# Performance work log

Hardware: AMD Instinct MI355X
Metric: run time of the kernel (lower is better)

## Reference

```python
import jax, jax.numpy as jnp
import numpy as np


def setup_inputs() -> dict:
    key = jax.random.key(0)
    ks = jax.random.split(key, 8)
    B, De, Do, T, H, W = 4, 128, 512, 4, 30, 52
    s = 0.05  # weight init scale
    return {
        "m_in": jax.random.normal(ks[0], (B, De, T, H, W), jnp.float32),
        "m_out": jax.random.normal(ks[1], (B, Do, T, H, W), jnp.float32),
        "q_in": jax.random.normal(ks[2], (B, De, H, W), jnp.float32),
        "q_out": jax.random.normal(ks[3], (B, Do, H, W), jnp.float32),
        "wr": jax.random.normal(ks[4], (Do, 2 * Do), jnp.float32) * s,
        "br": jnp.zeros((Do,), jnp.float32),
        "wu": jax.random.normal(ks[5], (Do, 2 * Do), jnp.float32) * s,
        "bu": jnp.zeros((Do,), jnp.float32),
        "wc": jax.random.normal(ks[6], (Do, 2 * Do), jnp.float32) * s,
        "bc": jnp.zeros((Do,), jnp.float32),
    }


def reference(m_in, m_out, q_in, q_out, wr, br, wu, bu, wc, bc):
    B, De, T, H, W = m_in.shape
    Do = m_out.shape[1]
    PROP_LAYERS = 5

    # --- memory read: pairwise frame attention (bmm + softmax + bmm) ---
    # keys: all T memory frames flattened; queries: current frame.
    mi = m_in.reshape(B, De, T * H * W)            # [B, De, THW]
    qi = q_in.reshape(B, De, H * W)                # [B, De, HW]
    p = jnp.einsum('bdk,bdq->bkq', mi, qi) / (De ** 0.5)  # [B, THW, HW]
    p = jax.nn.softmax(p, axis=1)                  # softmax over memory locations (dim=1 in torch)
    mem = jnp.einsum('bok,bkq->boq', m_out.reshape(B, Do, T * H * W), p)
    mem = mem.reshape(B, Do, H, W)                 # mem_mean; identical every propagate layer

    # --- ConvGRU_h (kernel_size=1 => per-pixel linear gates) ---
    def conv1x1(w, b, x):
        return jnp.einsum('oc,bchw->bohw', w, x) + b[None, :, None, None]

    def gru(x, h):
        xh = jnp.concatenate([x, h], axis=1)                       # [B, 2*Do, H, W]
        r = jax.nn.sigmoid(conv1x1(wr, br, xh))
        u = jax.nn.sigmoid(conv1x1(wu, bu, xh))
        c = jnp.tanh(conv1x1(wc, bc, jnp.concatenate([x, r * h], axis=1)))
        return h * (1.0 - u) + u * c

    q0 = q_out
    q = q_out
    for _ in range(PROP_LAYERS):
        q = gru(q, mem)  # original: q_out = ConvGRU_h(q_out, mem_mean)
    return jnp.concatenate([q, q0], axis=1)  # [B, 2*Do, H, W]
```

## Files before the change

kernel.cpp:

```cpp
#include <hip/hip_runtime.h>
#include <hip/hip_bf16.h>
#include <math.h>

typedef unsigned short u16;
typedef __attribute__((ext_vector_type(8))) short bf16x8;
typedef __attribute__((ext_vector_type(4))) float f32x4;

__device__ __forceinline__ u16 f2bf(float f) {
  union { float f; unsigned u; } x; x.f = f;
  unsigned r = x.u + 0x7fffu + ((x.u >> 16) & 1u);
  return (u16)(r >> 16);
}
__device__ __forceinline__ float bf2f(u16 h) {
  union { unsigned u; float f; } x; x.u = ((unsigned)h) << 16;
  return x.f;
}
__device__ __forceinline__ float sigmf(float x) {
  x = fminf(fmaxf(x, -30.f), 30.f);
  return 1.f / (1.f + __expf(-x));
}
__device__ __forceinline__ float tanh_fast(float x) {
  x = fminf(fmaxf(x, -15.f), 15.f);
  float t = __expf(2.f * x);
  return (t - 1.f) / (t + 1.f);
}

#define NB 4
#define DE 128
#define DO_ 512
#define HW 1560
#define THW 6240
#define NP 1664
#define KP 6272
#define PROP 5
#define PVSPLIT 7
#define PVKC 896

template<int MODE, int ROWS, int KTOT>
__global__ __launch_bounds__(256)
void gemm_ws(const u16* __restrict__ A, const u16* __restrict__ Bt,
             int lda, int ldb, long a_bs, long b_bs,
             void* __restrict__ out0v, long o0_bs, int ld0,
             u16* __restrict__ out1, long o1_bs, int ld1,
             const void* __restrict__ e0v, long e0_bs,
             const void* __restrict__ e1v, long e1_bs,
             const void* __restrict__ e2v, long e2_bs,
             int nvalid, float scale)
{
  constexpr int MF = ROWS / 16;
  constexpr int SLOTS = ROWS * KTOT / 8;
  constexpr int NLD = SLOTS / 256;
  constexpr int RSH = (ROWS == 64) ? 6 : 5;
  __shared__ u16 lds[SLOTS][8];

  const int tid = threadIdx.x;
  const int wave = tid >> 6, lane = tid & 63;
  const int kg = lane >> 4, lr = lane & 15;
  const long b = blockIdx.z;
  const int m0 = blockIdx.x * ROWS, n0 = blockIdx.y * 128;
  A += b * a_bs; Bt += b * b_bs;

  float* out0f = (float*)out0v;
  u16* out0h = (u16*)out0v;
  const float* e0f = (const float*)e0v;
  const u16* e0h = (const u16*)e0v;
  const u16* e1h = (const u16*)e1v;
  const u16* e2h = (const u16*)e2v;

#pragma unroll
  for (int i = 0; i < NLD; ++i) {
    int s = tid + 256 * i;
    int row = s & (ROWS - 1), g = s >> RSH;
    const u16* src = A + (long)(m0 + row) * lda + g * 8;
    __builtin_amdgcn_global_load_lds(
        (const __attribute__((address_space(1))) void*)src,
        (__attribute__((address_space(3))) void*)&lds[wave * 64 + 256 * i][0],
        16, 0, 0);
  }
  __syncthreads();

  f32x4 acc[MF][2];
#pragma unroll
  for (int m = 0; m < MF; ++m)
#pragma unroll
    for (int n = 0; n < 2; ++n) acc[m][n] = (f32x4){0.f, 0.f, 0.f, 0.f};

  const u16* Bp0 = Bt + (long)(n0 + wave * 32 + lr) * ldb + kg * 8;
  const u16* Bp1 = Bp0 + 16 * ldb;

  constexpr int NK = KTOT / 32;
#pragma unroll 4
  for (int g2 = 0; g2 < NK; ++g2) {
    bf16x8 af[MF], bf[2];
#pragma unroll
    for (int m = 0; m < MF; ++m)
      af[m] = *(const bf16x8*)&lds[(g2 * 4 + kg) * ROWS + m * 16 + lr][0];
    bf[0] = *(const bf16x8*)&Bp0[g2 * 32];
    bf[1] = *(const bf16x8*)&Bp1[g2 * 32];
#pragma unroll
    for (int m = 0; m < MF; ++m)
#pragma unroll
      for (int n = 0; n < 2; ++n)
        acc[m][n] = __builtin_amdgcn_mfma_f32_16x16x32_bf16(af[m], bf[n], acc[m][n], 0, 0, 0);
  }

  if constexpr (MODE == 0) {
    float rs[MF][4];
#pragma unroll
    for (int m = 0; m < MF; ++m)
#pragma unroll
      for (int j = 0; j < 4; ++j) rs[m][j] = 0.f;
#pragma unroll
    for (int m = 0; m < MF; ++m) {
#pragma unroll
      for (int n = 0; n < 2; ++n) {
        int col = n0 + wave * 32 + n * 16 + lr;
#pragma unroll
        for (int j = 0; j < 4; ++j) {
          long row = m0 + m * 16 + kg * 4 + j;
          float p = __expf(acc[m][n][j] * scale);
          bool valid = (col < nvalid);
          out1[b * o1_bs + row * ld1 + col] = valid ? f2bf(p) : (u16)0;
          rs[m][j] += valid ? p : 0.f;
        }
      }
    }
#pragma unroll
    for (int m = 0; m < MF; ++m)
#pragma unroll
      for (int j = 0; j < 4; ++j) {
#pragma unroll
        for (int msk = 1; msk < 16; msk <<= 1)
          rs[m][j] += __shfl_xor(rs[m][j], msk, 64);
      }
    __syncthreads();
    float* zbuf = (float*)&lds[0][0];
    if (lr == 0) {
#pragma unroll
      for (int m = 0; m < MF; ++m)
#pragma unroll
        for (int j = 0; j < 4; ++j)
          zbuf[wave * 64 + m * 16 + kg * 4 + j] = rs[m][j];
    }
    __syncthreads();
    if (tid < 64)
      out0f[b * o0_bs + (long)blockIdx.y * NP + (m0 + tid)] =
          zbuf[tid] + zbuf[64 + tid] + zbuf[128 + tid] + zbuf[192 + tid];
    return;
  }

#pragma unroll
  for (int m = 0; m < MF; ++m) {
#pragma unroll
    for (int n = 0; n < 2; ++n) {
      int col = n0 + wave * 32 + n * 16 + lr;
#pragma unroll
      for (int j = 0; j < 4; ++j) {
        long row = m0 + m * 16 + kg * 4 + j;
        float v = acc[m][n][j];
        if constexpr (MODE == 2) {
          out1[b * o1_bs + row * ld1 + col] = f2bf(v + e0f[col]);
        } else if constexpr (MODE == 3) {
          float gt = sigmf(v + bf2f(e0h[b * e0_bs + row * 1024 + col]));
          if (col < 512)
            out1[b * o1_bs + row * ld1 + 512 + col] =
                f2bf(gt * bf2f(e1h[b * e1_bs + row * 512 + col]));
          else
            out0h[b * o0_bs + row * ld0 + (col - 512)] = f2bf(gt);
        } else if constexpr (MODE == 4) {
          float cg = tanh_fast(v + e0f[col]);
          float u = bf2f(e1h[b * e1_bs + row * 512 + col]);
          float mm = bf2f(e2h[b * e2_bs + row * 512 + col]);
          float x = mm * (1.f - u) + u * cg;
          out1[b * o1_bs + row * ld1 + col] = f2bf(x);
          if (out0f) out0f[b * o0_bs + row * ld0 + col] = x;
        }
      }
    }
  }
}

__global__ __launch_bounds__(256, 2)
void gemm_pv(const u16* __restrict__ Pt, const u16* __restrict__ moutb,
             u16* __restrict__ Ppart)
{
  const int m0 = blockIdx.x * 64;
  const int z = blockIdx.y;
  const int b = blockIdx.z;
  const int k0 = z * PVKC;

  const u16* A = Pt + (long)b * NP * KP;
  const u16* B0;
  {
    const u16* Bb = moutb + (long)b * DO_ * KP;
    B0 = Bb + (long)((threadIdx.x >> 6) * 128 + (threadIdx.x & 15)) * KP +
         ((threadIdx.x & 63) >> 4) * 8;
  }

  __shared__ u16 lds[2][2048];
  const int tid = threadIdx.x;
  const int wave = tid >> 6, lane = tid & 63;
  const int kg = lane >> 4, lr = lane & 15;

  auto stage = [&](int buf, int kt) {
    int row = tid & 63, g = tid >> 6;
    const u16* src = A + (long)(m0 + row) * KP + kt + g * 8;
    __builtin_amdgcn_global_load_lds(
        (const __attribute__((address_space(1))) void*)src,
        (__attribute__((address_space(3))) void*)&lds[buf][(wave * 64) * 8],
        16, 0, 0);
  };

  f32x4 acc[4][8];
#pragma unroll
  for (int m = 0; m < 4; ++m)
#pragma unroll
    for (int n = 0; n < 8; ++n) acc[m][n] = (f32x4){0.f, 0.f, 0.f, 0.f};

  bf16x8 bra[8], brb[8];
#pragma unroll
  for (int n = 0; n < 8; ++n)
    bra[n] = *(const bf16x8*)&B0[(long)n * 16 * KP + k0];
  stage(0, k0);
  __syncthreads();

#define PV_STEP(BU, BL, T, CUR)                                                  \
  {                                                                              \
    if ((T) + 1 < 28) {                                                          \
      int ktn = k0 + ((T) + 1) * 32;                                             \
      _Pragma("unroll") for (int n = 0; n < 8; ++n)                              \
          BL[n] = *(const bf16x8*)&B0[(long)n * 16 * KP + ktn];                  \
      stage((CUR) ^ 1, ktn);                                                     \
    }                                                                            \
    bf16x8 af[4];                                                                \
    _Pragma("unroll") for (int m = 0; m < 4; ++m)                                \
        af[m] = *(const bf16x8*)&lds[CUR][(kg * 64 + m * 16 + lr) * 8];          \
    _Pragma("unroll") for (int m = 0; m < 4; ++m)                                \
        _Pragma("unroll") for (int n = 0; n < 8; ++n)                            \
            acc[m][n] = __builtin_amdgcn_mfma_f32_16x16x32_bf16(af[m], BU[n],    \
                                                                acc[m][n], 0, 0, 0); \
    __syncthreads();                                                             \
  }

  for (int tp = 0; tp < 14; ++tp) {
    PV_STEP(bra, brb, 2 * tp, 0);
    PV_STEP(brb, bra, 2 * tp + 1, 1);
  }
#undef PV_STEP

  u16* out = Ppart + (long)(b * PVSPLIT + z) * NP * DO_;
#pragma unroll
  for (int m = 0; m < 4; ++m) {
#pragma unroll
    for (int n = 0; n < 8; ++n) {
      int col = wave * 128 + n * 16 + lr;
#pragma unroll
      for (int j = 0; j < 4; ++j) {
        int row = m0 + m * 16 + kg * 4 + j;
        out[(long)row * DO_ + col] = f2bf(acc[m][n][j]);
      }
    }
  }
}

__global__ void k_transpose_cast(const float* __restrict__ in, u16* __restrict__ out,
                                 int R, int C, int Cp, int out_ld,
                                 long in_bs, long out_bs) {
  __shared__ float t[32][33];
  long b = blockIdx.z;
  int c0 = blockIdx.x * 32, r0 = blockIdx.y * 32;
  int tx = threadIdx.x, ty = threadIdx.y;
#pragma unroll
  for (int i = 0; i < 32; i += 8) {
    int r = r0 + ty + i, c = c0 + tx;
    t[ty + i][tx] = (r < R && c < C) ? in[b * in_bs + (long)r * C + c] : 0.f;
  }
  __syncthreads();
#pragma unroll
  for (int i = 0; i < 32; i += 8) {
    int c = c0 + ty + i, r = r0 + tx;
    if (c < Cp && r < R)
      out[b * out_bs + (long)c * out_ld + r] = f2bf(t[tx][ty + i]);
  }
}

__global__ void k_cast_pad(const float* __restrict__ in, u16* __restrict__ out,
                           int Cin, int Cout, long in_bs, long out_bs) {
  int c = blockIdx.x * 256 + threadIdx.x;
  int r = blockIdx.y;
  long b = blockIdx.z;
  if (c >= Cout) return;
  out[b * out_bs + (long)r * Cout + c] =
      (c < Cin) ? f2bf(in[b * in_bs + (long)r * Cin + c]) : (u16)0;
}

__global__ void k_build_wru(const float* __restrict__ wr_, const float* __restrict__ wu_,
                            u16* __restrict__ wrux, u16* __restrict__ wruh) {
  int k = blockIdx.x * 256 + threadIdx.x;
  int m = blockIdx.y;
  if (k >= 512) return;
  const float* src = (m < 512) ? wr_ : wu_;
  int mm = m & 511;
  wrux[m * 512 + k] = f2bf(src[mm * 1024 + k]);
  wruh[m * 512 + k] = f2bf(src[mm * 1024 + 512 + k]);
}

__global__ void k_bias_ru(const float* __restrict__ br_, const float* __restrict__ bu_,
                          float* __restrict__ bias) {
  int i = blockIdx.x * 256 + threadIdx.x;
  if (i < 1024) bias[i] = (i < 512) ? br_[i] : bu_[i - 512];
}

__global__ void k_invz(const float* __restrict__ Zp, float* __restrict__ invZ) {
  int t = blockIdx.x * 256 + threadIdx.x;
  if (t >= NB * NP) return;
  int b = t / NP, q = t - b * NP;
  const float* base = Zp + (long)b * 49 * NP + q;
  float s = 0.f;
#pragma unroll
  for (int nb = 0; nb < 49; ++nb) s += base[(long)nb * NP];
  invZ[t] = 1.f / s;
}

__global__ void k_reduce_mem(const u16* __restrict__ Ppart, const float* __restrict__ invZ,
                             u16* __restrict__ memTb) {
  long t = (long)blockIdx.x * 256 + threadIdx.x;
  const long bs = (long)NP * DO_;
  if (t >= (long)NB * bs / 8) return;
  long flat = t * 8;
  int b = (int)(flat / bs);
  long r = flat - (long)b * bs;
  int q = (int)(r / DO_);
  float s[8];
#pragma unroll
  for (int e = 0; e < 8; ++e) s[e] = 0.f;
#pragma unroll
  for (int z = 0; z < PVSPLIT; ++z) {
    uint4 v = *(const uint4*)&Ppart[(long)(b * PVSPLIT + z) * bs + r];
    s[0] += bf2f((u16)(v.x & 0xffff)); s[1] += bf2f((u16)(v.x >> 16));
    s[2] += bf2f((u16)(v.y & 0xffff)); s[3] += bf2f((u16)(v.y >> 16));
    s[4] += bf2f((u16)(v.z & 0xffff)); s[5] += bf2f((u16)(v.z >> 16));
    s[6] += bf2f((u16)(v.w & 0xffff)); s[7] += bf2f((u16)(v.w >> 16));
  }
  float iz = invZ[b * NP + q];
  uint4 o;
  o.x = (unsigned)f2bf(s[0] * iz) | ((unsigned)f2bf(s[1] * iz) << 16);
  o.y = (unsigned)f2bf(s[2] * iz) | ((unsigned)f2bf(s[3] * iz) << 16);
  o.z = (unsigned)f2bf(s[4] * iz) | ((unsigned)f2bf(s[5] * iz) << 16);
  o.w = (unsigned)f2bf(s[6] * iz) | ((unsigned)f2bf(s[7] * iz) << 16);
  *(uint4*)&memTb[(long)b * bs + r] = o;
}

__global__ void k_out_q(const float* __restrict__ Qfin, float* __restrict__ dout) {
  __shared__ float t[32][33];
  long b = blockIdx.z;
  int q0 = blockIdx.x * 32, ch0 = blockIdx.y * 32;
  int tx = threadIdx.x, ty = threadIdx.y;
#pragma unroll
  for (int i = 0; i < 32; i += 8)
    t[ty + i][tx] = Qfin[b * ((long)NP * 512) + (long)(q0 + ty + i) * 512 + ch0 + tx];
  __syncthreads();
#pragma unroll
  for (int i = 0; i < 32; i += 8) {
    int ch = ch0 + ty + i, q = q0 + tx;
    if (q < HW)
      dout[b * ((long)1024 * HW) + (long)ch * HW + q] = t[tx][ty + i];
  }
}

__global__ void k_copy_q0(const float4* __restrict__ src, float4* __restrict__ dst) {
  int idx = blockIdx.x * 256 + threadIdx.x;
  long b = blockIdx.z;
  const long n4 = (long)DO_ * HW / 4;
  if (idx < n4)
    dst[b * ((long)1024 * HW / 4) + n4 + idx] = src[b * n4 + idx];
}

extern "C" void kernel_launch(void* const* d_in, const int* in_sizes, int n_in,
                              void* d_out, int out_size, void* d_ws, size_t ws_size,
                              hipStream_t stream) {
  const float* m_in  = (const float*)d_in[0];
  const float* m_out = (const float*)d_in[1];
  const float* q_in  = (const float*)d_in[2];
  const float* q_out = (const float*)d_in[3];
  const float* wr    = (const float*)d_in[4];
  const float* br    = (const float*)d_in[5];
  const float* wu    = (const float*)d_in[6];
  const float* bu    = (const float*)d_in[7];
  const float* wc    = (const float*)d_in[8];
  const float* bc    = (const float*)d_in[9];
  float* dout = (float*)d_out;

  char* p = (char*)d_ws;
  size_t off = 0;
  auto alloc = [&](size_t bytes) { void* r = p + off; off += (bytes + 255) & ~(size_t)255; return r; };
  u16*   miT    = (u16*)alloc((size_t)NB * KP * DE * 2);
  u16*   qiT    = (u16*)alloc((size_t)NB * NP * DE * 2);
  u16*   Pt     = (u16*)alloc((size_t)NB * NP * KP * 2);
  float* invZ   = (float*)alloc((size_t)NB * NP * 4);
  u16*   moutb  = (u16*)alloc((size_t)NB * DO_ * KP * 2);
  u16*   memTb  = (u16*)alloc((size_t)NB * NP * DO_ * 2);
  u16*   chru   = (u16*)alloc((size_t)NB * NP * 1024 * 2);
  u16*   U      = (u16*)alloc((size_t)NB * NP * DO_ * 2);
  u16*   XRb    = (u16*)alloc((size_t)NB * NP * 1024 * 2);
  float* Qfin   = (float*)alloc((size_t)NB * NP * DO_ * 4);
  u16*   XRa    = (u16*)alloc((size_t)NB * NP * 1024 * 2);
  u16*   wrux   = (u16*)alloc((size_t)1024 * 512 * 2);
  u16*   wruh   = (u16*)alloc((size_t)1024 * 512 * 2);
  u16*   wcb    = (u16*)alloc((size_t)512 * 1024 * 2);
  float* biasru = (float*)alloc((size_t)1024 * 4);
  u16*   Ppart  = (u16*)chru;
  float* Zp     = (float*)memTb;
  if (off > ws_size) return;

  k_build_wru<<<dim3(2, 1024), 256, 0, stream>>>(wr, wu, wrux, wruh);
  k_cast_pad<<<dim3(4, 512, 1), 256, 0, stream>>>(wc, wcb, 1024, 1024, 0, 0);
  k_bias_ru<<<dim3(4), 256, 0, stream>>>(br, bu, biasru);
  k_cast_pad<<<dim3(25, 512, NB), 256, 0, stream>>>(
      m_out, moutb, THW, KP, (long)DO_ * THW, (long)DO_ * KP);
  k_transpose_cast<<<dim3(196, 4, NB), dim3(32, 8), 0, stream>>>(
      m_in, miT, DE, THW, KP, DE, (long)DE * THW, (long)KP * DE);
  k_transpose_cast<<<dim3(52, 4, NB), dim3(32, 8), 0, stream>>>(
      q_in, qiT, DE, HW, NP, DE, (long)DE * HW, (long)NP * DE);
  k_transpose_cast<<<dim3(52, 16, NB), dim3(32, 8), 0, stream>>>(
      q_out, XRa, DO_, HW, NP, 1024, (long)DO_ * HW, (long)NP * 1024);

  gemm_ws<0, 64, 128><<<dim3(26, 49, NB), 256, 0, stream>>>(
      qiT, miT, DE, DE, (long)NP * DE, (long)KP * DE,
      Zp, (long)49 * NP, 0, Pt, (long)NP * KP, KP,
      nullptr, 0, nullptr, 0, nullptr, 0, THW, 0.08838834764831845f);
  k_invz<<<dim3(26), 256, 0, stream>>>(Zp, invZ);

  gemm_pv<<<dim3(26, PVSPLIT, NB), 256, 0, stream>>>(Pt, moutb, Ppart);
  k_reduce_mem<<<dim3(1664), 256, 0, stream>>>(Ppart, invZ, memTb);

  gemm_ws<2, 64, 512><<<dim3(26, 8, NB), 256, 0, stream>>>(
      memTb, wruh, DO_, DO_, (long)NP * DO_, 0,
      nullptr, 0, 0, chru, (long)NP * 1024, 1024,
      biasru, 0, nullptr, 0, nullptr, 0, 0, 0.f);

  u16* xr[2] = {XRa, XRb};
  for (int l = 0; l < PROP; ++l) {
    u16* cur = xr[l & 1];
    u16* nxt = xr[(l + 1) & 1];
    gemm_ws<3, 64, 512><<<dim3(26, 8, NB), 256, 0, stream>>>(
        cur, wrux, 1024, DO_, (long)NP * 1024, 0,
        U, (long)NP * DO_, DO_, cur, (long)NP * 1024, 1024,
        chru, (long)NP * 1024, memTb, (long)NP * DO_, nullptr, 0, 0, 0.f);
    gemm_ws<4, 32, 1024><<<dim3(52, 4, NB), 256, 0, stream>>>(
        cur, wcb, 1024, 1024, (long)NP * 1024, 0,
        (l == PROP - 1) ? (void*)Qfin : nullptr, (long)NP * DO_, DO_,
        nxt, (long)NP * 1024, 1024,
        bc, 0, U, (long)NP * DO_, memTb, (long)NP * DO_, 0, 0.f);
  }

  k_out_q<<<dim3(49, 16, NB), dim3(32, 8), 0, stream>>>(Qfin, dout);
  k_copy_q0<<<dim3(780, 1, NB), 256, 0, stream>>>((const float4*)q_out, (float4*)dout);
}
```

Measured before the change: 745.8 us.

## Fuse all GRU propagation layers into one persistent LDS-resident kernel

Replaces the ten per-layer gate and candidate GEMM launches with a single gru_fused kernel. Each block keeps its 64-row tile of the hidden state and r*h in swizzled LDS across all five layers, and reads weights pre-arranged into MFMA fragment order by a new k_wfrag kernel. The PV GEMM launch is flattened to a 1D grid with an XCD-aware block remap, and the score GEMM is specialised into its own kernel. The aim is to cut launch overhead and the global round-trips of intermediate activations. The cost is that only 104 large blocks run, which leaves many CUs idle and gives low occupancy.

```diff
diff --git a/kernel.cpp b/kernel.cpp
--- a/kernel.cpp
+++ b/kernel.cpp
@@ -36,42 +36,24 @@
 #define PVSPLIT 7
 #define PVKC 896
 
-template<int MODE, int ROWS, int KTOT>
 __global__ __launch_bounds__(256)
-void gemm_ws(const u16* __restrict__ A, const u16* __restrict__ Bt,
-             int lda, int ldb, long a_bs, long b_bs,
-             void* __restrict__ out0v, long o0_bs, int ld0,
-             u16* __restrict__ out1, long o1_bs, int ld1,
-             const void* __restrict__ e0v, long e0_bs,
-             const void* __restrict__ e1v, long e1_bs,
-             const void* __restrict__ e2v, long e2_bs,
-             int nvalid, float scale)
+void gemm_scores(const u16* __restrict__ qiT, const u16* __restrict__ miT,
+                 float* __restrict__ Zp, u16* __restrict__ Pt)
 {
-  constexpr int MF = ROWS / 16;
-  constexpr int SLOTS = ROWS * KTOT / 8;
-  constexpr int NLD = SLOTS / 256;
-  constexpr int RSH = (ROWS == 64) ? 6 : 5;
-  __shared__ u16 lds[SLOTS][8];
-
+  __shared__ u16 lds[1024][8];
   const int tid = threadIdx.x;
   const int wave = tid >> 6, lane = tid & 63;
   const int kg = lane >> 4, lr = lane & 15;
   const long b = blockIdx.z;
-  const int m0 = blockIdx.x * ROWS, n0 = blockIdx.y * 128;
-  A += b * a_bs; Bt += b * b_bs;
-
-  float* out0f = (float*)out0v;
-  u16* out0h = (u16*)out0v;
-  const float* e0f = (const float*)e0v;
-  const u16* e0h = (const u16*)e0v;
-  const u16* e1h = (const u16*)e1v;
-  const u16* e2h = (const u16*)e2v;
-
-#pragma unroll
-  for (int i = 0; i < NLD; ++i) {
+  const int m0 = blockIdx.x * 64, n0 = blockIdx.y * 128;
+  const u16* A = qiT + b * ((long)NP * DE);
+  const u16* Bt = miT + b * ((long)KP * DE);
+
+#pragma unroll
+  for (int i = 0; i < 4; ++i) {
     int s = tid + 256 * i;
-    int row = s & (ROWS - 1), g = s >> RSH;
-    const u16* src = A + (long)(m0 + row) * lda + g * 8;
+    int row = s & 63, g = s >> 6;
+    const u16* src = A + (long)(m0 + row) * DE + g * 8;
     __builtin_amdgcn_global_load_lds(
         (const __attribute__((address_space(1))) void*)src,
         (__attribute__((address_space(3))) void*)&lds[wave * 64 + 256 * i][0],
@@ -79,114 +61,83 @@
   }
   __syncthreads();
 
-  f32x4 acc[MF][2];
-#pragma unroll
-  for (int m = 0; m < MF; ++m)
+  f32x4 acc[4][2];
+#pragma unroll
+  for (int m = 0; m < 4; ++m)
 #pragma unroll
     for (int n = 0; n < 2; ++n) acc[m][n] = (f32x4){0.f, 0.f, 0.f, 0.f};
 
-  const u16* Bp0 = Bt + (long)(n0 + wave * 32 + lr) * ldb + kg * 8;
-  const u16* Bp1 = Bp0 + 16 * ldb;
-
-  constexpr int NK = KTOT / 32;
-#pragma unroll 4
-  for (int g2 = 0; g2 < NK; ++g2) {
-    bf16x8 af[MF], bf[2];
-#pragma unroll
-    for (int m = 0; m < MF; ++m)
-      af[m] = *(const bf16x8*)&lds[(g2 * 4 + kg) * ROWS + m * 16 + lr][0];
+  const u16* Bp0 = Bt + (long)(n0 + wave * 32 + lr) * DE + kg * 8;
+  const u16* Bp1 = Bp0 + 16 * DE;
+#pragma unroll
+  for (int g2 = 0; g2 < 4; ++g2) {
+    bf16x8 af[4], bf[2];
+#pragma unroll
+    for (int m = 0; m < 4; ++m)
+      af[m] = *(const bf16x8*)&lds[(g2 * 4 + kg) * 64 + m * 16 + lr][0];
     bf[0] = *(const bf16x8*)&Bp0[g2 * 32];
     bf[1] = *(const bf16x8*)&Bp1[g2 * 32];
 #pragma unroll
-    for (int m = 0; m < MF; ++m)
+    for (int m = 0; m < 4; ++m)
 #pragma unroll
       for (int n = 0; n < 2; ++n)
         acc[m][n] = __builtin_amdgcn_mfma_f32_16x16x32_bf16(af[m], bf[n], acc[m][n], 0, 0, 0);
   }
 
-  if constexpr (MODE == 0) {
-    float rs[MF][4];
-#pragma unroll
-    for (int m = 0; m < MF; ++m)
-#pragma unroll
-      for (int j = 0; j < 4; ++j) rs[m][j] = 0.f;
-#pragma unroll
-    for (int m = 0; m < MF; ++m) {
-#pragma unroll
-      for (int n = 0; n < 2; ++n) {
-        int col = n0 + wave * 32 + n * 16 + lr;
-#pragma unroll
-        for (int j = 0; j < 4; ++j) {
-          long row = m0 + m * 16 + kg * 4 + j;
-          float p = __expf(acc[m][n][j] * scale);
-          bool valid = (col < nvalid);
-          out1[b * o1_bs + row * ld1 + col] = valid ? f2bf(p) : (u16)0;
-          rs[m][j] += valid ? p : 0.f;
-        }
-      }
-    }
-#pragma unroll
-    for (int m = 0; m < MF; ++m)
-#pragma unroll
-      for (int j = 0; j < 4; ++j) {
-#pragma unroll
-        for (int msk = 1; msk < 16; msk <<= 1)
-          rs[m][j] += __shfl_xor(rs[m][j], msk, 64);
-      }
-    __syncthreads();
-    float* zbuf = (float*)&lds[0][0];
-    if (lr == 0) {
-#pragma unroll
-      for (int m = 0; m < MF; ++m)
-#pragma unroll
-        for (int j = 0; j < 4; ++j)
-          zbuf[wave * 64 + m * 16 + kg * 4 + j] = rs[m][j];
-    }
-    __syncthreads();
-    if (tid < 64)
-      out0f[b * o0_bs + (long)blockIdx.y * NP + (m0 + tid)] =
-          zbuf[tid] + zbuf[64 + tid] + zbuf[128 + tid] + zbuf[192 + tid];
-    return;
-  }
-
-#pragma unroll
-  for (int m = 0; m < MF; ++m) {
+  const float scale = 0.08838834764831845f;
+  float rs[4][4];
+#pragma unroll
+  for (int m = 0; m < 4; ++m)
+#pragma unroll
+    for (int j = 0; j < 4; ++j) rs[m][j] = 0.f;
+#pragma unroll
+  for (int m = 0; m < 4; ++m) {
 #pragma unroll
     for (int n = 0; n < 2; ++n) {
       int col = n0 + wave * 32 + n * 16 + lr;
 #pragma unroll
       for (int j = 0; j < 4; ++j) {
         long row = m0 + m * 16 + kg * 4 + j;
-        float v = acc[m][n][j];
-        if constexpr (MODE == 2) {
-          out1[b * o1_bs + row * ld1 + col] = f2bf(v + e0f[col]);
-        } else if constexpr (MODE == 3) {
-          float gt = sigmf(v + bf2f(e0h[b * e0_bs + row * 1024 + col]));
-          if (col < 512)
-            out1[b * o1_bs + row * ld1 + 512 + col] =
-                f2bf(gt * bf2f(e1h[b * e1_bs + row * 512 + col]));
-          else
-            out0h[b * o0_bs + row * ld0 + (col - 512)] = f2bf(gt);
-        } else if constexpr (MODE == 4) {
-          float cg = tanh_fast(v + e0f[col]);
-          float u = bf2f(e1h[b * e1_bs + row * 512 + col]);
-          float mm = bf2f(e2h[b * e2_bs + row * 512 + col]);
-          float x = mm * (1.f - u) + u * cg;
-          out1[b * o1_bs + row * ld1 + col] = f2bf(x);
-          if (out0f) out0f[b * o0_bs + row * ld0 + col] = x;
-        }
+        float p = __expf(acc[m][n][j] * scale);
+        bool valid = (col < THW);
+        Pt[b * ((long)NP * KP) + row * KP + col] = valid ? f2bf(p) : (u16)0;
+        rs[m][j] += valid ? p : 0.f;
       }
     }
   }
+#pragma unroll
+  for (int m = 0; m < 4; ++m)
+#pragma unroll
+    for (int j = 0; j < 4; ++j) {
+#pragma unroll
+      for (int msk = 1; msk < 16; msk <<= 1)
+        rs[m][j] += __shfl_xor(rs[m][j], msk, 64);
+    }
+  __syncthreads();
+  float* zbuf = (float*)&lds[0][0];
+  if (lr == 0) {
+#pragma unroll
+    for (int m = 0; m < 4; ++m)
+#pragma unroll
+      for (int j = 0; j < 4; ++j)
+        zbuf[wave * 64 + m * 16 + kg * 4 + j] = rs[m][j];
+  }
+  __syncthreads();
+  if (tid < 64)
+    Zp[b * ((long)49 * NP) + (long)blockIdx.y * NP + (m0 + tid)] =
+        zbuf[tid] + zbuf[64 + tid] + zbuf[128 + tid] + zbuf[192 + tid];
 }
 
 __global__ __launch_bounds__(256, 2)
 void gemm_pv(const u16* __restrict__ Pt, const u16* __restrict__ moutb,
              u16* __restrict__ Ppart)
 {
-  const int m0 = blockIdx.x * 64;
-  const int z = blockIdx.y;
-  const int b = blockIdx.z;
+  const int bid = blockIdx.x;
+  const int xcd = bid & 7, i = bid >> 3;
+  const int s = xcd * 91 + i;
+  const int pair = s / 26, mb = s - pair * 26;
+  const int b = pair / PVSPLIT, z = pair - b * PVSPLIT;
+  const int m0 = mb * 64;
   const int k0 = z * PVKC;
 
   const u16* A = Pt + (long)b * NP * KP;
@@ -263,6 +214,187 @@
   }
 }
 
+__global__ __launch_bounds__(512, 2)
+void gru_fused(const u16* __restrict__ qT, const u16* __restrict__ memTb,
+               const u16* __restrict__ Wfu, const u16* __restrict__ Wfr,
+               const u16* __restrict__ Wfuh, const u16* __restrict__ Wfrh,
+               const u16* __restrict__ Wfc,
+               const float* __restrict__ br_, const float* __restrict__ bu_,
+               const float* __restrict__ bc_,
+               u16* __restrict__ chru, float* __restrict__ Qfin)
+{
+  __shared__ u16 xs[64 * 512];
+  __shared__ u16 rhs[64 * 512];
+  const int tid = threadIdx.x;
+  const int wave = tid >> 6, lane = tid & 63;
+  const int kg = lane >> 4, lr = lane & 15;
+  const int b = blockIdx.y;
+  const int m0 = blockIdx.x * 64;
+
+  const u16* qs = qT + ((long)b * NP + m0) * 512;
+  const u16* msp = memTb + ((long)b * NP + m0) * 512;
+  u16* chp = chru + ((long)b * NP + m0) * 1024;
+
+#pragma unroll
+  for (int i = 0; i < 8; ++i) {
+    int s = tid + 512 * i;
+    int row = s >> 6, k8 = (s & 63) * 8;
+    int di = row * 512 + (k8 ^ ((row & 7) << 3));
+    *(uint4*)&xs[di] = *(const uint4*)&qs[row * 512 + k8];
+    *(uint4*)&rhs[di] = *(const uint4*)&msp[row * 512 + k8];
+  }
+  __syncthreads();
+
+  f32x4 au[4][4], ar[4][4];
+
+#define GATES_LOOP(SRC, WU, WR)                                                 \
+  _Pragma("unroll")                                                             \
+  for (int m = 0; m < 4; ++m)                                                   \
+    _Pragma("unroll")                                                           \
+    for (int nf = 0; nf < 4; ++nf) {                                            \
+      au[m][nf] = (f32x4){0.f, 0.f, 0.f, 0.f};                                  \
+      ar[m][nf] = (f32x4){0.f, 0.f, 0.f, 0.f};                                  \
+    }                                                                           \
+  _Pragma("unroll 2")                                                           \
+  for (int kt = 0; kt < 16; ++kt) {                                             \
+    bf16x8 af[4], wu4[4], wr4[4];                                               \
+    _Pragma("unroll")                                                           \
+    for (int m = 0; m < 4; ++m) {                                               \
+      int row = m * 16 + lr;                                                    \
+      af[m] = *(const bf16x8*)&SRC[row * 512 +                                  \
+                                   ((kt * 32 + kg * 8) ^ ((row & 7) << 3))];    \
+    }                                                                           \
+    _Pragma("unroll")                                                           \
+    for (int nf = 0; nf < 4; ++nf) {                                            \
+      long wo = (long)((kt * 32 + wave * 4 + nf) * 512 + lane * 8);             \
+      wu4[nf] = *(const bf16x8*)&WU[wo];                                        \
+      wr4[nf] = *(const bf16x8*)&WR[wo];                                        \
+    }                                                                           \
+    _Pragma("unroll")                                                           \
+    for (int m = 0; m < 4; ++m)                                                 \
+      _Pragma("unroll")                                                         \
+      for (int nf = 0; nf < 4; ++nf) {                                          \
+        au[m][nf] = __builtin_amdgcn_mfma_f32_16x16x32_bf16(af[m], wu4[nf],     \
+                                                            au[m][nf], 0, 0, 0); \
+        ar[m][nf] = __builtin_amdgcn_mfma_f32_16x16x32_bf16(af[m], wr4[nf],     \
+                                                            ar[m][nf], 0, 0, 0); \
+      }                                                                         \
+  }
+
+  GATES_LOOP(rhs, Wfuh, Wfrh);
+#pragma unroll
+  for (int m = 0; m < 4; ++m)
+#pragma unroll
+    for (int nf = 0; nf < 4; ++nf) {
+      int col = wave * 64 + nf * 16 + lr;
+#pragma unroll
+      for (int j = 0; j < 4; ++j) {
+        int row = m * 16 + kg * 4 + j;
+        chp[(long)row * 1024 + col] = f2bf(ar[m][nf][j] + br_[col]);
+        chp[(long)row * 1024 + 512 + col] = f2bf(au[m][nf][j] + bu_[col]);
+      }
+    }
+  __syncthreads();
+
+  for (int l = 0; l < PROP; ++l) {
+    GATES_LOOP(xs, Wfu, Wfr);
+    unsigned u_pk[4][4][2];
+#pragma unroll
+    for (int m = 0; m < 4; ++m)
+#pragma unroll
+      for (int nf = 0; nf < 4; ++nf) {
+        int col = wave * 64 + nf * 16 + lr;
+#pragma unroll
+        for (int p = 0; p < 2; ++p) {
+          int r0 = m * 16 + kg * 4 + 2 * p;
+          float uu0 = sigmf(au[m][nf][2 * p] + bf2f(chp[(long)r0 * 1024 + 512 + col]));
+          float uu1 = sigmf(au[m][nf][2 * p + 1] + bf2f(chp[(long)(r0 + 1) * 1024 + 512 + col]));
+          u_pk[m][nf][p] = (unsigned)f2bf(uu0) | ((unsigned)f2bf(uu1) << 16);
+          float rr0 = sigmf(ar[m][nf][2 * p] + bf2f(chp[(long)r0 * 1024 + col]));
+          float rr1 = sigmf(ar[m][nf][2 * p + 1] + bf2f(chp[(long)(r0 + 1) * 1024 + col]));
+          float h0 = bf2f(msp[(long)r0 * 512 + col]);
+          float h1 = bf2f(msp[(long)(r0 + 1) * 512 + col]);
+          rhs[r0 * 512 + (col ^ ((r0 & 7) << 3))] = f2bf(rr0 * h0);
+          rhs[(r0 + 1) * 512 + (col ^ (((r0 + 1) & 7) << 3))] = f2bf(rr1 * h1);
+        }
+      }
+    __syncthreads();
+
+    f32x4 ac[4][4];
+#pragma unroll
+    for (int m = 0; m < 4; ++m)
+#pragma unroll
+      for (int nf = 0; nf < 4; ++nf) ac[m][nf] = (f32x4){0.f, 0.f, 0.f, 0.f};
+#pragma unroll 2
+    for (int kt = 0; kt < 16; ++kt) {
+      bf16x8 af[4], wf4[4];
+#pragma unroll
+      for (int m = 0; m < 4; ++m) {
+        int row = m * 16 + lr;
+        af[m] = *(const bf16x8*)&xs[row * 512 + ((kt * 32 + kg * 8) ^ ((row & 7) << 3))];
+      }
+#pragma unroll
+      for (int nf = 0; nf < 4; ++nf)
+        wf4[nf] = *(const bf16x8*)&Wfc[(long)((kt * 32 + wave * 4 + nf) * 512 + lane * 8)];
+#pragma unroll
+      for (int m = 0; m < 4; ++m)
+#pragma unroll
+        for (int nf = 0; nf < 4; ++nf)
+          ac[m][nf] = __builtin_amdgcn_mfma_f32_16x16x32_bf16(af[m], wf4[nf], ac[m][nf], 0, 0, 0);
+    }
+#pragma unroll 2
+    for (int kt = 0; kt < 16; ++kt) {
+      bf16x8 af[4], wf4[4];
+#pragma unroll
+      for (int m = 0; m < 4; ++m) {
+        int row = m * 16 + lr;
+        af[m] = *(const bf16x8*)&rhs[row * 512 + ((kt * 32 + kg * 8) ^ ((row & 7) << 3))];
+      }
+#pragma unroll
+      for (int nf = 0; nf < 4; ++nf)
+        wf4[nf] = *(const bf16x8*)&Wfc[(long)(((kt + 16) * 32 + wave * 4 + nf) * 512 + lane * 8)];
+#pragma unroll
+      for (int m = 0; m < 4; ++m)
+#pragma unroll
+        for (int nf = 0; nf < 4; ++nf)
+          ac[m][nf] = __builtin_amdgcn_mfma_f32_16x16x32_bf16(af[m], wf4[nf], ac[m][nf], 0, 0, 0);
+    }
+    __syncthreads();
+
+#pragma unroll
+    for (int m = 0; m < 4; ++m)
+#pragma unroll
+      for (int nf = 0; nf < 4; ++nf) {
+        int col = wave * 64 + nf * 16 + lr;
+#pragma unroll
+        for (int j = 0; j < 4; ++j) {
+          int row = m * 16 + kg * 4 + j;
+          float cg = tanh_fast(ac[m][nf][j] + bc_[col]);
+          u16 uh = (u16)((j & 1) ? (u_pk[m][nf][j >> 1] >> 16)
+                                 : (u_pk[m][nf][j >> 1] & 0xffff));
+          float uu = bf2f(uh);
+          float h = bf2f(msp[(long)row * 512 + col]);
+          float xn = h * (1.f - uu) + uu * cg;
+          if (l == PROP - 1)
+            Qfin[((long)b * NP + m0 + row) * 512 + col] = xn;
+          else
+            xs[row * 512 + (col ^ ((row & 7) << 3))] = f2bf(xn);
+        }
+      }
+    if (l < PROP - 1) __syncthreads();
+  }
+#undef GATES_LOOP
+}
+
+__global__ void k_wfrag(const float* __restrict__ src, u16* __restrict__ dst,
+                        int Ksrc, int koff) {
+  int t = blockIdx.x * 256 + threadIdx.x;
+  int e = t & 7, lane = (t >> 3) & 63, nb = (t >> 9) & 31, kt = t >> 14;
+  int n = nb * 16 + (lane & 15);
+  int k = koff + kt * 32 + (lane >> 4) * 8 + e;
+  dst[t] = f2bf(src[(long)n * Ksrc + k]);
+}
+
 __global__ void k_transpose_cast(const float* __restrict__ in, u16* __restrict__ out,
                                  int R, int C, int Cp, int out_ld,
                                  long in_bs, long out_bs) {
@@ -292,23 +424,6 @@
   if (c >= Cout) return;
   out[b * out_bs + (long)r * Cout + c] =
       (c < Cin) ? f2bf(in[b * in_bs + (long)r * Cin + c]) : (u16)0;
-}
-
-__global__ void k_build_wru(const float* __restrict__ wr_, const float* __restrict__ wu_,
-                            u16* __restrict__ wrux, u16* __restrict__ wruh) {
-  int k = blockIdx.x * 256 + threadIdx.x;
-  int m = blockIdx.y;
-  if (k >= 512) return;
-  const float* src = (m < 512) ? wr_ : wu_;
-  int mm = m & 511;
-  wrux[m * 512 + k] = f2bf(src[mm * 1024 + k]);
-  wruh[m * 512 + k] = f2bf(src[mm * 1024 + 512 + k]);
-}
-
-__global__ void k_bias_ru(const float* __restrict__ br_, const float* __restrict__ bu_,
-                          float* __restrict__ bias) {
-  int i = blockIdx.x * 256 + threadIdx.x;
-  if (i < 1024) bias[i] = (i < 512) ? br_[i] : bu_[i - 512];
 }
 
 __global__ void k_invz(const float* __restrict__ Zp, float* __restrict__ invZ) {
@@ -401,21 +516,22 @@
   u16*   moutb  = (u16*)alloc((size_t)NB * DO_ * KP * 2);
   u16*   memTb  = (u16*)alloc((size_t)NB * NP * DO_ * 2);
   u16*   chru   = (u16*)alloc((size_t)NB * NP * 1024 * 2);
-  u16*   U      = (u16*)alloc((size_t)NB * NP * DO_ * 2);
-  u16*   XRb    = (u16*)alloc((size_t)NB * NP * 1024 * 2);
-  float* Qfin   = (float*)alloc((size_t)NB * NP * DO_ * 4);
-  u16*   XRa    = (u16*)alloc((size_t)NB * NP * 1024 * 2);
-  u16*   wrux   = (u16*)alloc((size_t)1024 * 512 * 2);
-  u16*   wruh   = (u16*)alloc((size_t)1024 * 512 * 2);
-  u16*   wcb    = (u16*)alloc((size_t)512 * 1024 * 2);
-  float* biasru = (float*)alloc((size_t)1024 * 4);
-  u16*   Ppart  = (u16*)chru;
+  u16*   qT     = (u16*)alloc((size_t)NB * NP * 512 * 2);
+  float* Qfin   = (float*)alloc((size_t)NB * NP * 512 * 4);
+  u16*   Ppart  = (u16*)alloc((size_t)NB * PVSPLIT * NP * DO_ * 2);
+  u16*   Wfu    = (u16*)alloc((size_t)512 * 512 * 2);
+  u16*   Wfr    = (u16*)alloc((size_t)512 * 512 * 2);
+  u16*   Wfuh   = (u16*)alloc((size_t)512 * 512 * 2);
+  u16*   Wfrh   = (u16*)alloc((size_t)512 * 512 * 2);
+  u16*   Wfc    = (u16*)alloc((size_t)512 * 1024 * 2);
   float* Zp     = (float*)memTb;
   if (off > ws_size) return;
 
-  k_build_wru<<<dim3(2, 1024), 256, 0, stream>>>(wr, wu, wrux, wruh);
-  k_cast_pad<<<dim3(4, 512, 1), 256, 0, stream>>>(wc, wcb, 1024, 1024, 0, 0);
-  k_bias_ru<<<dim3(4), 256, 0, stream>>>(br, bu, biasru);
+  k_wfrag<<<dim3(1024), 256, 0, stream>>>(wu, Wfu, 1024, 0);
+  k_wfrag<<<dim3(1024), 256, 0, stream>>>(wr, Wfr, 1024, 0);
+  k_wfrag<<<dim3(1024), 256, 0, stream>>>(wu, Wfuh, 1024, 512);
+  k_wfrag<<<dim3(1024), 256, 0, stream>>>(wr, Wfrh, 1024, 512);
+  k_wfrag<<<dim3(2048), 256, 0, stream>>>(wc, Wfc, 1024, 0);
   k_cast_pad<<<dim3(25, 512, NB), 256, 0, stream>>>(
       m_out, moutb, THW, KP, (long)DO_ * THW, (long)DO_ * KP);
   k_transpose_cast<<<dim3(196, 4, NB), dim3(32, 8), 0, stream>>>(
@@ -423,36 +539,16 @@
   k_transpose_cast<<<dim3(52, 4, NB), dim3(32, 8), 0, stream>>>(
       q_in, qiT, DE, HW, NP, DE, (long)DE * HW, (long)NP * DE);
   k_transpose_cast<<<dim3(52, 16, NB), dim3(32, 8), 0, stream>>>(
-      q_out, XRa, DO_, HW, NP, 1024, (long)DO_ * HW, (long)NP * 1024);
-
-  gemm_ws<0, 64, 128><<<dim3(26, 49, NB), 256, 0, stream>>>(
-      qiT, miT, DE, DE, (long)NP * DE, (long)KP * DE,
-      Zp, (long)49 * NP, 0, Pt, (long)NP * KP, KP,
-      nullptr, 0, nullptr, 0, nullptr, 0, THW, 0.08838834764831845f);
+      q_out, qT, DO_, HW, NP, 512, (long)DO_ * HW, (long)NP * 512);
+
+  gemm_scores<<<dim3(26, 49, NB), 256, 0, stream>>>(qiT, miT, Zp, Pt);
   k_invz<<<dim3(26), 256, 0, stream>>>(Zp, invZ);
 
-  gemm_pv<<<dim3(26, PVSPLIT, NB), 256, 0, stream>>>(Pt, moutb, Ppart);
+  gemm_pv<<<dim3(728), 256, 0, stream>>>(Pt, moutb, Ppart);
   k_reduce_mem<<<dim3(1664), 256, 0, stream>>>(Ppart, invZ, memTb);
 
-  gemm_ws<2, 64, 512><<<dim3(26, 8, NB), 256, 0, stream>>>(
-      memTb, wruh, DO_, DO_, (long)NP * DO_, 0,
-      nullptr, 0, 0, chru, (long)NP * 1024, 1024,
-      biasru, 0, nullptr, 0, nullptr, 0, 0, 0.f);
-
-  u16* xr[2] = {XRa, XRb};
-  for (int l = 0; l < PROP; ++l) {
-    u16* cur = xr[l & 1];
-    u16* nxt = xr[(l + 1) & 1];
-    gemm_ws<3, 64, 512><<<dim3(26, 8, NB), 256, 0, stream>>>(
-        cur, wrux, 1024, DO_, (long)NP * 1024, 0,
-        U, (long)NP * DO_, DO_, cur, (long)NP * 1024, 1024,
-        chru, (long)NP * 1024, memTb, (long)NP * DO_, nullptr, 0, 0, 0.f);
-    gemm_ws<4, 32, 1024><<<dim3(52, 4, NB), 256, 0, stream>>>(
-        cur, wcb, 1024, 1024, (long)NP * 1024, 0,
-        (l == PROP - 1) ? (void*)Qfin : nullptr, (long)NP * DO_, DO_,
-        nxt, (long)NP * 1024, 1024,
-        bc, 0, U, (long)NP * DO_, memTb, (long)NP * DO_, 0, 0.f);
-  }
+  gru_fused<<<dim3(26, NB), 512, 0, stream>>>(
+      qT, memTb, Wfu, Wfr, Wfuh, Wfrh, Wfc, br, bu, bc, chru, Qfin);
 
   k_out_q<<<dim3(49, 16, NB), dim3(32, 8), 0, stream>>>(Qfin, dout);
   k_copy_q0<<<dim3(780, 1, NB), 256, 0, stream>>>((const float4*)q_out, (float4*)dout);
```

Result: no change. 756.9 us (+1.5%).
